# Optimization experiments

Hardware: AMD Instinct MI355X
Metric: run time of the kernel (lower is better)

The kernel has to match this reference:

```python
import jax, jax.numpy as jnp
import numpy as np

B, N, CIN, H, D, K = 8, 1000, 16, 64, 16, 3  # batch, nodes, in_dim, hidden, embed_dim, cheb_k
XIN = CIN + H  # GRU concat input dim


def setup_inputs() -> dict:
    key = jax.random.key(0)
    ks = jax.random.split(key, 18)
    f = lambda k, s, sc=1.0: jax.random.normal(k, s, dtype=jnp.float32) * sc
    inp = {}
    inp['x1'] = f(ks[0], (B, N, CIN)); inp['x2'] = f(ks[1], (B, N, CIN)); inp['x3'] = f(ks[2], (B, N, CIN))
    inp['state1'] = f(ks[3], (B, N, H)); inp['state2'] = f(ks[4], (B, N, H)); inp['state3'] = f(ks[5], (B, N, H))
    for i, name in enumerate(['support1', 'support2', 'support3']):
        a = jax.random.uniform(ks[6 + i], (N, N), dtype=jnp.float32)
        inp[name] = a / a.sum(-1, keepdims=True)  # row-stochastic graph, keeps Chebyshev stable
    inp['embeddings1'] = f(ks[9], (N, D), 0.1); inp['embeddings2'] = f(ks[10], (N, D), 0.1); inp['embeddings3'] = f(ks[11], (N, D), 0.1)
    inp['mode_embedding'] = f(ks[12], (3, D), 0.5)
    # xavier-normal-ish scales for the hypernet weight pools
    inp['Wg'] = f(ks[13], (D, K * XIN, 2 * H), (2.0 / (K * XIN * 2 * H + D * 2 * H)) ** 0.5)
    inp['Bg'] = f(ks[14], (D, 2 * H), (2.0 / (D + 2 * H)) ** 0.5)
    inp['Wu'] = f(ks[15], (D, K * XIN, H), (2.0 / (K * XIN * H + D * H)) ** 0.5)
    inp['Bu'] = f(ks[16], (D, H), (2.0 / (D + H)) ** 0.5)
    return inp


def _cheb_gcn(x, support, emb, wp, bp):
    # x:[B,N,C], support:[N,N], emb:[N,D], wp:[D,K*C,O], bp:[D,O]
    # Chebyshev recurrence applied directly to features (equivalent to building T_k(support))
    terms = [x, jnp.einsum('nm,bmc->bnc', support, x)]
    for _ in range(2, K):
        terms.append(2.0 * jnp.einsum('nm,bmc->bnc', support, terms[-1]) - terms[-2])
    x_g = jnp.concatenate(terms, axis=-1)  # [B,N,K*C]
    # meta_axis='S': per-node weights = emb @ wp ; fused contraction
    out = jnp.einsum('bni,nd,dio->bno', x_g, emb, wp) + emb @ bp  # [B,N,O]
    return out


def _cell(x, state, support, emb, me, Wg, Bg, Wu, Bu):
    # me:[D] mode embedding scales the shared pools (einsum 'mc,cdf->mcdf' -> pick mode m)
    zr = jax.nn.sigmoid(_cheb_gcn(jnp.concatenate([x, state], -1), support, emb,
                                  me[:, None, None] * Wg, me[:, None] * Bg))
    z, r = jnp.split(zr, 2, axis=-1)
    hc = jnp.tanh(_cheb_gcn(jnp.concatenate([x, z * state], -1), support, emb,
                            me[:, None, None] * Wu, me[:, None] * Bu))
    return r * state + (1.0 - r) * hc


def reference(x1, x2, x3, state1, state2, state3, support1, support2, support3,
              embeddings1, embeddings2, embeddings3, mode_embedding, Wg, Bg, Wu, Bu):
    h1 = _cell(x1, state1, support1, embeddings1, mode_embedding[0], Wg, Bg, Wu, Bu)
    h2 = _cell(x2, state2, support2, embeddings2, mode_embedding[1], Wg, Bg, Wu, Bu)
    h3 = _cell(x3, state3, support3, embeddings3, mode_embedding[2], Wg, Bg, Wu, Bu)
    return (h1, h2, h3)
```

## Files before the change

kernel.cpp:

```cpp
#include <hip/hip_runtime.h>
#include <math.h>


typedef __attribute__((ext_vector_type(8))) short s16x8;
typedef __attribute__((ext_vector_type(4))) float f32x4;
typedef unsigned short u16;
typedef unsigned int u32;
typedef unsigned long long u64;

__device__ __forceinline__ u32 f2bf(float f) {
  union { float f; u32 u; } v; v.f = f;
  return (v.u + 0x7FFFu + ((v.u >> 16) & 1u)) >> 16;
}
__device__ __forceinline__ float bf2f(u16 h) {
  union { u32 u; float f; } v; v.u = (u32)h << 16; return v.f;
}
__device__ __forceinline__ u64 pk4(float a, float b, float c, float d) {
  return (u64)f2bf(a) | ((u64)f2bf(b) << 16) | ((u64)f2bf(c) << 32) |
         ((u64)f2bf(d) << 48);
}
__device__ __forceinline__ void glds16(const u16* g, u16* l) {
  __builtin_amdgcn_global_load_lds(
      (const __attribute__((address_space(1))) void*)g,
      (__attribute__((address_space(3))) void*)l, 16, 0, 0);
}

#define E0 3145728
#define E1 1966080
#define E2 1920000
#define E3 384000
#define E4 384000
#define E5 384000
#define E6 119808

struct PrepAuxArgs {
  const float* x[3]; const float* st[3]; const float* S[3];
  u16 *S16, *Xt, *Ag, *AgU, *T1t, *ZSt, *SZ1t;
  const float *e0, *e1, *e2, *me, *Bg, *Bu, *Wg, *Wu;
  float *BiG, *BiU; u16 *BtG, *BtU;
};

__global__ void prep_aux(PrepAuxArgs P) {
  long tid = (long)blockIdx.x * 256 + threadIdx.x;
  if (tid < 2075904) {
    long idx = tid * 4;
    if (idx < E0) {
      int m = (int)(idx >> 20); int rem = (int)(idx & 1048575);
      int n = rem >> 10, k = rem & 1023;
      u64 pv = 0;
      if (n < 1000 && k < 1000) {
        f32x4 v = *(const f32x4*)&P.S[m][n * 1000 + k];
        pv = pk4(v[0], v[1], v[2], v[3]);
      }
      *(u64*)&P.S16[(size_t)m * 1048576 + rem] = pv; return;
    }
    idx -= E0;
    if (idx < E1) {
      int m = (int)(idx / 655360); int rem = (int)(idx % 655360);
      int col = rem >> 10, nn = rem & 1023;
      int b = col / 80, c = col % 80;
      u64 pv = 0;
      if (nn < 1000) {
        float f[4];
#pragma unroll
        for (int j = 0; j < 4; ++j)
          f[j] = (c < 16) ? P.x[m][(b * 1000 + nn + j) * 16 + c]
                          : P.st[m][(b * 1000 + nn + j) * 64 + c - 16];
        pv = pk4(f[0], f[1], f[2], f[3]);
      }
      *(u64*)&P.Xt[(size_t)m * 655360 + rem] = pv; return;
    }
    idx -= E1;
    if (idx < E2) {
      int m = (int)(idx / 640000); int rem = (int)(idx % 640000);
      int r = rem / 80, c = rem % 80;
      int n = r >> 3, b = r & 7;
      f32x4 v = (c < 16) ? *(const f32x4*)&P.x[m][(b * 1000 + n) * 16 + c]
                         : *(const f32x4*)&P.st[m][(b * 1000 + n) * 64 + c - 16];
      *(u64*)&P.Ag[(size_t)m * 2048000 + (size_t)r * 256 + c] =
          pk4(v[0], v[1], v[2], v[3]);
      return;
    }
    idx -= E2;
    if (idx < E3) {
      int m = (int)(idx / 128000); int rem = (int)(idx % 128000);
      int r = rem / 16, c = 240 + rem % 16;
      *(u64*)&P.Ag[(size_t)m * 2048000 + (size_t)r * 256 + c] = 0; return;
    }
    idx -= E3;
    if (idx < E4) {
      int m = (int)(idx / 128000); int rem = (int)(idx % 128000);
      int r = rem / 16, c = rem % 16;
      int n = r >> 3, b = r & 7;
      f32x4 v = *(const f32x4*)&P.x[m][(b * 1000 + n) * 16 + c];
      *(u64*)&P.AgU[(size_t)m * 2048000 + (size_t)r * 256 + c] =
          pk4(v[0], v[1], v[2], v[3]);
      return;
    }
    idx -= E4;
    if (idx < E5) {
      int m = (int)(idx / 128000); int rem = (int)(idx % 128000);
      int r = rem / 16, c = 240 + rem % 16;
      *(u64*)&P.AgU[(size_t)m * 2048000 + (size_t)r * 256 + c] = 0; return;
    }
    idx -= E5;
    if (idx < E6) {
      int m = (int)(idx / 39936); int rem = (int)(idx % 39936);
      if (rem < 15360) { int col = rem / 24, j = rem % 24;
        *(u64*)&P.T1t[(size_t)m * 655360 + col * 1024 + 1000 + j] = 0; }
      else if (rem < 27648) { int e = rem - 15360; int col = e / 24, j = e % 24;
        *(u64*)&P.ZSt[(size_t)m * 524288 + col * 1024 + 1000 + j] = 0; }
      else { int e = rem - 27648; int col = e / 24, j = e % 24;
        *(u64*)&P.SZ1t[(size_t)m * 524288 + col * 1024 + 1000 + j] = 0; }
      return;
    }
    return;
  }
  int idx = (int)(tid - 2075904);
  if (idx < 384000) {
    int mode = idx / 128000, rem = idx % 128000;
    int n = rem >> 7, o = rem & 127;
    const float* emb = (mode == 0) ? P.e0 : (mode == 1) ? P.e1 : P.e2;
    float s = 0.f;
#pragma unroll
    for (int d = 0; d < 16; ++d)
      s += emb[n * 16 + d] * P.me[mode * 16 + d] * P.Bg[d * 128 + o];
    P.BiG[idx] = s; return;
  }
  idx -= 384000;
  if (idx < 192000) {
    int mode = idx / 64000, rem = idx % 64000;
    int n = rem >> 6, o = rem & 63;
    const float* emb = (mode == 0) ? P.e0 : (mode == 1) ? P.e1 : P.e2;
    float s = 0.f;
#pragma unroll
    for (int d = 0; d < 16; ++d)
      s += emb[n * 16 + d] * P.me[mode * 16 + d] * P.Bu[d * 64 + o];
    P.BiU[idx] = s; return;
  }
  idx -= 192000;
  if (idx < 524288) {
    int col = idx >> 8, k = idx & 255;
    int d = col >> 7, o = col & 127;
    P.BtG[idx] = (k < 240) ? (u16)f2bf(P.Wg[d * 30720 + k * 128 + o]) : (u16)0;
    return;
  }
  idx -= 524288;
  if (idx < 262144) {
    int col = idx >> 8, k = idx & 255;
    int d = col >> 6, o = col & 63;
    P.BtU[idx] = (k < 240) ? (u16)f2bf(P.Wu[d * 15360 + k * 64 + o]) : (u16)0;
  }
}

struct ChebArgs2 {
  const u16* S16[3]; const u16* A[3]; const u16* Res[3];
  u16* Yt[3]; u16* AgA[3]; u16* AgX[3];
};

__global__ __launch_bounds__(256, 4) void cheb_v6(ChebArgs2 g, int fdiv, int agbase,
                                                  float alpha, float beta, int flags) {
  const int mode = blockIdx.z;
  const u16* __restrict__ Ab = g.A[mode];
  const u16* __restrict__ Sb = g.S16[mode];

  __shared__ u16 As[32 * 128];
  __shared__ u16 Bs[64 * 128];

  const int t = threadIdx.x;
  const int row0 = blockIdx.y * 32, n0 = blockIdx.x * 64;
  const int lane = t & 63, wid = t >> 6;
  const int l16 = lane & 15, quad = lane >> 4;
  const int wx = wid * 16;

  f32x4 acc[2];
#pragma unroll
  for (int a = 0; a < 2; ++a) acc[a] = (f32x4){0.f, 0.f, 0.f, 0.f};

  for (int k0 = 0; k0 < 1024; k0 += 128) {
#pragma unroll
    for (int p = 0; p < 2; ++p) {
      int idx = p * 256 + t; int row = idx >> 4; int cs = (idx & 15) ^ (row & 7);
      glds16(Ab + (size_t)(row0 + row) * 1024 + k0 + cs * 8, &As[idx * 8]);
    }
#pragma unroll
    for (int p = 0; p < 4; ++p) {
      int idx = p * 256 + t; int row = idx >> 4; int cs = (idx & 15) ^ (row & 7);
      glds16(Sb + (size_t)(n0 + row) * 1024 + k0 + cs * 8, &Bs[idx * 8]);
    }
    __syncthreads();
    s16x8 af[2][4], bf[4];
#pragma unroll
    for (int mi = 0; mi < 2; ++mi) {
      int row = mi * 16 + l16;
#pragma unroll
      for (int ks = 0; ks < 4; ++ks) {
        int cl = (ks * 4 + quad) ^ (row & 7);
        af[mi][ks] = *(const s16x8*)&As[row * 128 + cl * 8];
      }
    }
    {
      int row = wx + l16;
#pragma unroll
      for (int ks = 0; ks < 4; ++ks) {
        int cl = (ks * 4 + quad) ^ (row & 7);
        bf[ks] = *(const s16x8*)&Bs[row * 128 + cl * 8];
      }
    }
#pragma unroll
    for (int ks = 0; ks < 4; ++ks)
#pragma unroll
      for (int mi = 0; mi < 2; ++mi)
        acc[mi] = __builtin_amdgcn_mfma_f32_16x16x32_bf16(af[mi][ks], bf[ks], acc[mi], 0, 0, 0);
    __syncthreads();
  }

#pragma unroll
  for (int mi = 0; mi < 2; ++mi) {
    int frow0 = row0 + mi * 16 + quad * 4;
    int b = frow0 / fdiv, c0 = frow0 - b * fdiv;
    int n = n0 + wx + l16;
    if (n < 1000) {
      u16 pk[4];
#pragma unroll
      for (int r = 0; r < 4; ++r) {
        float v = alpha * acc[mi][r];
        if (flags & 1) v += beta * bf2f(g.Res[mode][(size_t)(frow0 + r) * 1024 + n]);
        u16 h = (u16)f2bf(v);
        pk[r] = h;
        if (flags & 2) g.Yt[mode][(size_t)(frow0 + r) * 1024 + n] = h;
      }
      u64 pv = (u64)pk[0] | ((u64)pk[1] << 16) | ((u64)pk[2] << 32) | ((u64)pk[3] << 48);
      *(u64*)&g.AgA[mode][(size_t)(n * 8 + b) * 256 + agbase + c0] = pv;
      if ((flags & 4) && c0 < 16)
        *(u64*)&g.AgX[mode][(size_t)(n * 8 + b) * 256 + agbase + c0] = pv;
    }
  }
}

struct Meta3Args {
  const u16* Ag;
  const u16* Bt;
  const float* emb[3];
  const float* me;
  const float* Bias;
  const float* state[3];
  u16* ZSt;
  u16* AgU;
  float* Rb;
  float* out;
};

__global__ __launch_bounds__(256, 4) void meta3(Meta3Args A, int is_gate, int O) {
  const int mode = blockIdx.z;
  const int row0 = blockIdx.y * 64;
  const int n0 = row0 >> 3;
  const int oc = blockIdx.x;
  const int ocbase = oc * 64;

  __shared__ u16 Bs[64 * 256];
  __shared__ float ewS[8][17];

  const int t = threadIdx.x;
  if (t < 128) {
    int nl = t >> 4, d = t & 15;
    ewS[nl][d] = A.emb[mode][(n0 + nl) * 16 + d] * A.me[mode * 16 + d];
  }

  const int lane = t & 63, wid = t >> 6;
  const int l16 = lane & 15, quad = lane >> 4;
  const int wy = (wid >> 1) * 32, wx = (wid & 1) * 32;
  const u16* Agm = A.Ag + (size_t)mode * 2048000;

#pragma unroll
  for (int p = 0; p < 8; ++p) {
    int idx = p * 256 + t; int row = idx >> 5; int cs = (idx & 31) ^ (row & 7);
    glds16(Agm + (size_t)(row0 + row) * 256 + cs * 8, &Bs[idx * 8]);
  }
  __syncthreads();

  s16x8 afr[2][8];
#pragma unroll
  for (int mi = 0; mi < 2; ++mi) {
    int row = wy + mi * 16 + l16;
#pragma unroll
    for (int ki = 0; ki < 8; ++ki) {
      int cl = (ki * 4 + quad) ^ (row & 7);
      afr[mi][ki] = *(const s16x8*)&Bs[row * 256 + cl * 8];
    }
  }
  __syncthreads();

  f32x4 outacc[2][2];
#pragma unroll
  for (int a = 0; a < 2; ++a)
#pragma unroll
    for (int b = 0; b < 2; ++b) outacc[a][b] = (f32x4){0.f, 0.f, 0.f, 0.f};

  for (int tl = 0; tl < 16; ++tl) {
    const int brow0 = tl * O + ocbase;
#pragma unroll
    for (int p = 0; p < 8; ++p) {
      int idx = p * 256 + t; int row = idx >> 5; int cs = (idx & 31) ^ (row & 7);
      glds16(A.Bt + (size_t)(brow0 + row) * 256 + cs * 8, &Bs[idx * 8]);
    }
    __syncthreads();

    f32x4 acc[2][2];
#pragma unroll
    for (int a = 0; a < 2; ++a)
#pragma unroll
      for (int b = 0; b < 2; ++b) acc[a][b] = (f32x4){0.f, 0.f, 0.f, 0.f};

#pragma unroll
    for (int ki = 0; ki < 8; ++ki) {
      s16x8 bfr[2];
#pragma unroll
      for (int ni = 0; ni < 2; ++ni) {
        int row = wx + ni * 16 + l16;
        int cl = (ki * 4 + quad) ^ (row & 7);
        bfr[ni] = *(const s16x8*)&Bs[row * 256 + cl * 8];
      }
#pragma unroll
      for (int mi = 0; mi < 2; ++mi)
#pragma unroll
        for (int ni = 0; ni < 2; ++ni)
          acc[mi][ni] = __builtin_amdgcn_mfma_f32_16x16x32_bf16(afr[mi][ki], bfr[ni], acc[mi][ni], 0, 0, 0);
    }

#pragma unroll
    for (int mi = 0; mi < 2; ++mi) {
      int nl = (wy + mi * 16 + quad * 4) >> 3;
      float s = ewS[nl][tl];
#pragma unroll
      for (int ni = 0; ni < 2; ++ni)
#pragma unroll
        for (int r = 0; r < 4; ++r)
          outacc[mi][ni][r] += s * acc[mi][ni][r];
    }
    __syncthreads();
  }

#pragma unroll
  for (int mi = 0; mi < 2; ++mi)
#pragma unroll
    for (int ni = 0; ni < 2; ++ni)
#pragma unroll
      for (int r = 0; r < 4; ++r) {
        int row = row0 + wy + mi * 16 + quad * 4 + r;
        int n = row >> 3, b = row & 7;
        int o = ocbase + wx + ni * 16 + l16;
        float pre = outacc[mi][ni][r] + A.Bias[(size_t)mode * 1000 * O + n * O + o];
        if (is_gate) {
          float sg = 1.f / (1.f + __expf(-pre));
          if (o < 64) {
            float st = A.state[mode][(b * 1000 + n) * 64 + o];
            float zs = sg * st;
            A.ZSt[(size_t)mode * 524288 + (size_t)(b * 64 + o) * 1024 + n] = (u16)f2bf(zs);
            A.AgU[(size_t)mode * 2048000 + (size_t)row * 256 + 16 + o] = (u16)f2bf(zs);
          } else {
            A.Rb[(size_t)mode * 512000 + row * 64 + (o - 64)] = sg;
          }
        } else {
          float hc = tanhf(pre);
          float rr = A.Rb[(size_t)mode * 512000 + row * 64 + o];
          float st = A.state[mode][(b * 1000 + n) * 64 + o];
          A.out[(size_t)mode * 512000 + (b * 1000 + n) * 64 + o] = rr * st + (1.f - rr) * hc;
        }
      }
}

extern "C" void kernel_launch(void* const* d_in, const int* in_sizes, int n_in,
                              void* d_out, int out_size, void* d_ws, size_t ws_size,
                              hipStream_t stream) {
  const float* x[3]   = {(const float*)d_in[0], (const float*)d_in[1], (const float*)d_in[2]};
  const float* st[3]  = {(const float*)d_in[3], (const float*)d_in[4], (const float*)d_in[5]};
  const float* S[3]   = {(const float*)d_in[6], (const float*)d_in[7], (const float*)d_in[8]};
  const float* emb[3] = {(const float*)d_in[9], (const float*)d_in[10], (const float*)d_in[11]};
  const float* me = (const float*)d_in[12];
  const float* Wg = (const float*)d_in[13];
  const float* Bg = (const float*)d_in[14];
  const float* Wu = (const float*)d_in[15];
  const float* Bu = (const float*)d_in[16];
  float* out = (float*)d_out;

  float* BiG = (float*)d_ws;
  float* BiU = BiG + 384000;
  float* Rb  = BiU + 192000;
  u16* S16 = (u16*)(Rb + 1536000);
  u16* Xt  = S16 + 3145728;
  u16* T1t = Xt + 1966080;
  u16* ZSt = T1t + 1966080;
  u16* SZ1t= ZSt + 1572864;
  u16* Ag  = SZ1t + 1572864;
  u16* AgU = Ag + 6144000;
  u16* BtG = AgU + 6144000;
  u16* BtU = BtG + 524288;

  {
    PrepAuxArgs P;
    for (int m = 0; m < 3; ++m) { P.x[m] = x[m]; P.st[m] = st[m]; P.S[m] = S[m]; }
    P.S16 = S16; P.Xt = Xt; P.Ag = Ag; P.AgU = AgU; P.T1t = T1t; P.ZSt = ZSt; P.SZ1t = SZ1t;
    P.e0 = emb[0]; P.e1 = emb[1]; P.e2 = emb[2]; P.me = me;
    P.Bg = Bg; P.Bu = Bu; P.Wg = Wg; P.Wu = Wu;
    P.BiG = BiG; P.BiU = BiU; P.BtG = BtG; P.BtU = BtU;
    prep_aux<<<13431, 256, 0, stream>>>(P);
  }

  {
    ChebArgs2 a;
    for (int m = 0; m < 3; ++m) {
      a.S16[m] = S16 + (size_t)m * 1048576; a.A[m] = Xt + (size_t)m * 655360;
      a.Res[m] = nullptr; a.Yt[m] = T1t + (size_t)m * 655360;
      a.AgA[m] = Ag + (size_t)m * 2048000; a.AgX[m] = AgU + (size_t)m * 2048000;
    }
    cheb_v6<<<dim3(16, 20, 3), 256, 0, stream>>>(a, 80, 80, 1.f, 0.f, 2 | 4);
  }
  {
    ChebArgs2 a;
    for (int m = 0; m < 3; ++m) {
      a.S16[m] = S16 + (size_t)m * 1048576; a.A[m] = T1t + (size_t)m * 655360;
      a.Res[m] = Xt + (size_t)m * 655360; a.Yt[m] = nullptr;
      a.AgA[m] = Ag + (size_t)m * 2048000; a.AgX[m] = AgU + (size_t)m * 2048000;
    }
    cheb_v6<<<dim3(16, 20, 3), 256, 0, stream>>>(a, 80, 160, 2.f, -1.f, 1 | 4);
  }
  {
    Meta3Args a;
    a.Ag = Ag; a.Bt = BtG; a.me = me; a.Bias = BiG;
    a.ZSt = ZSt; a.AgU = AgU; a.Rb = Rb; a.out = out;
    for (int m = 0; m < 3; ++m) { a.emb[m] = emb[m]; a.state[m] = st[m]; }
    meta3<<<dim3(2, 125, 3), 256, 0, stream>>>(a, 1, 128);
  }
  {
    ChebArgs2 a;
    for (int m = 0; m < 3; ++m) {
      a.S16[m] = S16 + (size_t)m * 1048576; a.A[m] = ZSt + (size_t)m * 524288;
      a.Res[m] = nullptr; a.Yt[m] = SZ1t + (size_t)m * 524288;
      a.AgA[m] = AgU + (size_t)m * 2048000; a.AgX[m] = nullptr;
    }
    cheb_v6<<<dim3(16, 16, 3), 256, 0, stream>>>(a, 64, 96, 1.f, 0.f, 2);
  }
  {
    ChebArgs2 a;
    for (int m = 0; m < 3; ++m) {
      a.S16[m] = S16 + (size_t)m * 1048576; a.A[m] = SZ1t + (size_t)m * 524288;
      a.Res[m] = ZSt + (size_t)m * 524288; a.Yt[m] = nullptr;
      a.AgA[m] = AgU + (size_t)m * 2048000; a.AgX[m] = nullptr;
    }
    cheb_v6<<<dim3(16, 16, 3), 256, 0, stream>>>(a, 64, 176, 2.f, -1.f, 1);
  }
  {
    Meta3Args a;
    a.Ag = AgU; a.Bt = BtU; a.me = me; a.Bias = BiU;
    a.ZSt = ZSt; a.AgU = AgU; a.Rb = Rb; a.out = out;
    for (int m = 0; m < 3; ++m) { a.emb[m] = emb[m]; a.state[m] = st[m]; }
    meta3<<<dim3(1, 125, 3), 256, 0, stream>>>(a, 0, 64);
  }
}
```

Before: 254.4 us.

## Split update meta contraction over embedding dim halves with separate epilogue

Result: no change. 249.5 us (-1.9%).

```diff
diff --git a/kernel.cpp b/kernel.cpp
--- a/kernel.cpp
+++ b/kernel.cpp
@@ -351,23 +351,136 @@
         int n = row >> 3, b = row & 7;
         int o = ocbase + wx + ni * 16 + l16;
         float pre = outacc[mi][ni][r] + A.Bias[(size_t)mode * 1000 * O + n * O + o];
-        if (is_gate) {
-          float sg = 1.f / (1.f + __expf(-pre));
-          if (o < 64) {
-            float st = A.state[mode][(b * 1000 + n) * 64 + o];
-            float zs = sg * st;
-            A.ZSt[(size_t)mode * 524288 + (size_t)(b * 64 + o) * 1024 + n] = (u16)f2bf(zs);
-            A.AgU[(size_t)mode * 2048000 + (size_t)row * 256 + 16 + o] = (u16)f2bf(zs);
-          } else {
-            A.Rb[(size_t)mode * 512000 + row * 64 + (o - 64)] = sg;
-          }
+        float sg = 1.f / (1.f + __expf(-pre));
+        if (o < 64) {
+          float st = A.state[mode][(b * 1000 + n) * 64 + o];
+          float zs = sg * st;
+          A.ZSt[(size_t)mode * 524288 + (size_t)(b * 64 + o) * 1024 + n] = (u16)f2bf(zs);
+          A.AgU[(size_t)mode * 2048000 + (size_t)row * 256 + 16 + o] = (u16)f2bf(zs);
         } else {
-          float hc = tanhf(pre);
-          float rr = A.Rb[(size_t)mode * 512000 + row * 64 + o];
-          float st = A.state[mode][(b * 1000 + n) * 64 + o];
-          A.out[(size_t)mode * 512000 + (b * 1000 + n) * 64 + o] = rr * st + (1.f - rr) * hc;
+          A.Rb[(size_t)mode * 512000 + row * 64 + (o - 64)] = sg;
         }
       }
+}
+
+__global__ __launch_bounds__(256, 4) void meta3u(Meta3Args A, float* Pacc) {
+  const int mode = blockIdx.z;
+  const int row0 = blockIdx.y * 64;
+  const int n0 = row0 >> 3;
+  const int dh = blockIdx.x;
+
+  __shared__ u16 Bs[64 * 256];
+  __shared__ float ewS[8][17];
+
+  const int t = threadIdx.x;
+  if (t < 128) {
+    int nl = t >> 4, d = t & 15;
+    ewS[nl][d] = A.emb[mode][(n0 + nl) * 16 + d] * A.me[mode * 16 + d];
+  }
+
+  const int lane = t & 63, wid = t >> 6;
+  const int l16 = lane & 15, quad = lane >> 4;
+  const int wy = (wid >> 1) * 32, wx = (wid & 1) * 32;
+  const u16* Agm = A.Ag + (size_t)mode * 2048000;
+
+#pragma unroll
+  for (int p = 0; p < 8; ++p) {
+    int idx = p * 256 + t; int row = idx >> 5; int cs = (idx & 31) ^ (row & 7);
+    glds16(Agm + (size_t)(row0 + row) * 256 + cs * 8, &Bs[idx * 8]);
+  }
+  __syncthreads();
+
+  s16x8 afr[2][8];
+#pragma unroll
+  for (int mi = 0; mi < 2; ++mi) {
+    int row = wy + mi * 16 + l16;
+#pragma unroll
+    for (int ki = 0; ki < 8; ++ki) {
+      int cl = (ki * 4 + quad) ^ (row & 7);
+      afr[mi][ki] = *(const s16x8*)&Bs[row * 256 + cl * 8];
+    }
+  }
+  __syncthreads();
+
+  f32x4 outacc[2][2];
+#pragma unroll
+  for (int a = 0; a < 2; ++a)
+#pragma unroll
+    for (int b = 0; b < 2; ++b) outacc[a][b] = (f32x4){0.f, 0.f, 0.f, 0.f};
+
+  for (int tl = dh * 8; tl < dh * 8 + 8; ++tl) {
+    const int brow0 = tl * 64;
+#pragma unroll
+    for (int p = 0; p < 8; ++p) {
+      int idx = p * 256 + t; int row = idx >> 5; int cs = (idx & 31) ^ (row & 7);
+      glds16(A.Bt + (size_t)(brow0 + row) * 256 + cs * 8, &Bs[idx * 8]);
+    }
+    __syncthreads();
+
+    f32x4 acc[2][2];
+#pragma unroll
+    for (int a = 0; a < 2; ++a)
+#pragma unroll
+      for (int b = 0; b < 2; ++b) acc[a][b] = (f32x4){0.f, 0.f, 0.f, 0.f};
+
+#pragma unroll
+    for (int ki = 0; ki < 8; ++ki) {
+      s16x8 bfr[2];
+#pragma unroll
+      for (int ni = 0; ni < 2; ++ni) {
+        int row = wx + ni * 16 + l16;
+        int cl = (ki * 4 + quad) ^ (row & 7);
+        bfr[ni] = *(const s16x8*)&Bs[row * 256 + cl * 8];
+      }
+#pragma unroll
+      for (int mi = 0; mi < 2; ++mi)
+#pragma unroll
+        for (int ni = 0; ni < 2; ++ni)
+          acc[mi][ni] = __builtin_amdgcn_mfma_f32_16x16x32_bf16(afr[mi][ki], bfr[ni], acc[mi][ni], 0, 0, 0);
+    }
+
+#pragma unroll
+    for (int mi = 0; mi < 2; ++mi) {
+      int nl = (wy + mi * 16 + quad * 4) >> 3;
+      float s = ewS[nl][tl];
+#pragma unroll
+      for (int ni = 0; ni < 2; ++ni)
+#pragma unroll
+        for (int r = 0; r < 4; ++r)
+          outacc[mi][ni][r] += s * acc[mi][ni][r];
+    }
+    __syncthreads();
+  }
+
+#pragma unroll
+  for (int mi = 0; mi < 2; ++mi)
+#pragma unroll
+    for (int ni = 0; ni < 2; ++ni)
+#pragma unroll
+      for (int r = 0; r < 4; ++r) {
+        int row = row0 + wy + mi * 16 + quad * 4 + r;
+        int o = wx + ni * 16 + l16;
+        Pacc[((size_t)(dh * 3 + mode) * 8000 + row) * 64 + o] = outacc[mi][ni][r];
+      }
+}
+
+__global__ void epi_u(const float* __restrict__ Pacc, const float* __restrict__ BiU,
+                      const float* __restrict__ Rb,
+                      const float* __restrict__ st0, const float* __restrict__ st1,
+                      const float* __restrict__ st2, float* __restrict__ out) {
+  int idx = blockIdx.x * blockDim.x + threadIdx.x;
+  if (idx >= 1536000) return;
+  int mode = idx / 512000, rem = idx % 512000;
+  int row = rem >> 6, o = rem & 63;
+  int n = row >> 3, b = row & 7;
+  float pre = Pacc[((size_t)mode * 8000 + row) * 64 + o] +
+              Pacc[((size_t)(3 + mode) * 8000 + row) * 64 + o] +
+              BiU[(size_t)mode * 64000 + n * 64 + o];
+  float hc = tanhf(pre);
+  float rr = Rb[(size_t)mode * 512000 + row * 64 + o];
+  const float* st = (mode == 0) ? st0 : (mode == 1) ? st1 : st2;
+  out[(size_t)mode * 512000 + (b * 1000 + n) * 64 + o] =
+      rr * st[(b * 1000 + n) * 64 + o] + (1.f - rr) * hc;
 }
 
 extern "C" void kernel_launch(void* const* d_in, const int* in_sizes, int n_in,
@@ -396,6 +509,7 @@
   u16* AgU = Ag + 6144000;
   u16* BtG = AgU + 6144000;
   u16* BtU = BtG + 524288;
+  float* PaccU = (float*)Ag;
 
   {
     PrepAuxArgs P;
@@ -455,6 +569,7 @@
     a.Ag = AgU; a.Bt = BtU; a.me = me; a.Bias = BiU;
     a.ZSt = ZSt; a.AgU = AgU; a.Rb = Rb; a.out = out;
     for (int m = 0; m < 3; ++m) { a.emb[m] = emb[m]; a.state[m] = st[m]; }
-    meta3<<<dim3(1, 125, 3), 256, 0, stream>>>(a, 0, 64);
-  }
-}
+    meta3u<<<dim3(2, 125, 3), 256, 0, stream>>>(a, PaccU);
+  }
+  epi_u<<<6000, 256, 0, stream>>>(PaccU, BiU, Rb, st[0], st[1], st[2], out);
+}
```
